# Optimization experiments

Hardware: AMD Instinct MI355X
Metric: run time of the kernel (lower is better)

Reference implementation:

```python
import jax, jax.numpy as jnp
import numpy as np

B, S, R, L, Z = 2048, 277, 80, 12, 56


def setup_inputs() -> dict:
    key = jax.random.key(0)
    k0, k1, k2, k3, k4, k5 = jax.random.split(key, 6)
    true_idx = jax.random.randint(k0, (B, S), 0, R)
    x = jax.nn.one_hot(true_idx, R, dtype=jnp.float32)            # one-hot true rules
    recon_x = jax.nn.softmax(jax.random.normal(k1, (B, S, R)), axis=-1)  # post-softmax probs
    mu = jax.random.normal(k2, (B, Z), dtype=jnp.float32)
    log_var = jax.random.normal(k3, (B, Z), dtype=jnp.float32)
    ind_to_lhs_ind = jax.random.randint(k4, (R,), 0, L)
    masks = (jax.random.uniform(k5, (L, R)) > 0.5).astype(jnp.float32)
    # a valid grammar always allows the true rule under its own LHS mask
    masks = masks.at[ind_to_lhs_ind, jnp.arange(R)].set(1.0)
    return {"x": x, "recon_x": recon_x, "mu": mu, "log_var": log_var,
            "masks": masks, "ind_to_lhs_ind": ind_to_lhs_ind}


def reference(x, recon_x, mu, log_var, masks, ind_to_lhs_ind):
    batch_size, seq_len, n_rules = x.shape
    z_size = mu.shape[1]
    # apply_masks: fused gather + mask + renormalize (replaces B*S python loop)
    true_rule = jnp.argmax(x, axis=-1)                 # [B,S]
    mask = masks[ind_to_lhs_ind[true_rule]]            # [B,S,R]
    x_resc = recon_x * mask
    out = x_resc / jnp.sum(x_resc, axis=-1, keepdims=True)
    # BCELoss(size_average=False): torch clamps log terms at -100
    log_p = jnp.clip(jnp.log(out), -100.0, None)
    log_1mp = jnp.clip(jnp.log1p(-out), -100.0, None)
    bce = -jnp.sum(x * log_p + (1.0 - x) * log_1mp) / (seq_len * batch_size)
    # sample_z == False branch: moment-matching error
    avg_mu = jnp.sum(mu, axis=0) / batch_size          # [Z]
    var = jnp.matmul(mu.T, mu) / batch_size            # [Z,Z]
    var_err = var - jnp.eye(z_size, dtype=mu.dtype)
    mom_err = jnp.sum(avg_mu * avg_mu) / z_size + jnp.sum(jnp.abs(var_err)) / (z_size * z_size)
    return bce + mom_err
```

## Files before the change

kernel.cpp:

```cpp
#include <hip/hip_runtime.h>
#include <math.h>

#define Bn 2048
#define Sn 277
#define Rn 80
#define Ln 12
#define Zn 56
#define NROWS (Bn * Sn)
#define ROWS_PER_BLK 64
#define NBLK_BCE (NROWS / ROWS_PER_BLK)
#define NMOM 32
#define MROWS (Bn / NMOM)
#define NBLK_TOT (NBLK_BCE + NMOM)

#define WS_CM  0
#define WS_BCE 1280
#define WS_VAR 36736
#define WS_AVG 49280

__device__ __forceinline__ float qsum4(float v) {
    int t = __builtin_amdgcn_update_dpp(0, __float_as_int(v), 0xB1, 0xF, 0xF, true);
    v += __int_as_float(t);
    t = __builtin_amdgcn_update_dpp(0, __float_as_int(v), 0x4E, 0xF, 0xF, true);
    v += __int_as_float(t);
    return v;
}

__global__ __launch_bounds__(256) void setup_kernel(
    const float* __restrict__ masks, const int* __restrict__ lhs, char* __restrict__ ws)
{
    unsigned* cmask_sw = (unsigned*)(ws + WS_CM);
    for (int idx = threadIdx.x; idx < Rn * 4; idx += 256) {
        const int r = idx >> 2, c = idx & 3;
        const int l = lhs[r];
        unsigned bits = 0u;
        for (int k = 0; k < 5; ++k)
            for (int comp = 0; comp < 4; ++comp) {
                const int j = 16 * k + 4 * c + comp;
                if (masks[l * Rn + j] > 0.5f) bits |= (1u << (4 * k + comp));
            }
        cmask_sw[idx] = bits;
    }
}

__global__ __launch_bounds__(256, 3) void main_kernel(
    const float* __restrict__ x, const float* __restrict__ recon,
    const float* __restrict__ mu, char* __restrict__ ws)
{
    __shared__ float4 ldsb[2688];
    const int tid = threadIdx.x;

    if (blockIdx.x < NMOM) {
        float* var_g = (float*)(ws + WS_VAR);
        float* avg_g = (float*)(ws + WS_AVG);
        float* sm = (float*)ldsb;
        const int m = blockIdx.x;
        const float* src = mu + (size_t)m * MROWS * Zn;
        for (int i = tid; i < MROWS * Zn; i += 256) sm[i] = src[i];
        __syncthreads();

        float acc[13];
        #pragma unroll
        for (int k = 0; k < 13; ++k) {
            const int p = tid + 256 * k;
            float a = 0.0f;
            if (p < Zn * Zn) {
                const int i = p / Zn, j = p - i * Zn;
                #pragma unroll 8
                for (int r = 0; r < MROWS; ++r) a = fmaf(sm[r * Zn + i], sm[r * Zn + j], a);
            }
            acc[k] = a;
        }
        #pragma unroll
        for (int k = 0; k < 13; ++k) {
            const int p = tid + 256 * k;
            if (p < Zn * Zn) atomicAdd(&var_g[p], acc[k]);
        }
        if (tid < Zn) {
            float s = 0.0f;
            #pragma unroll 8
            for (int r = 0; r < MROWS; ++r) s += sm[r * Zn + tid];
            atomicAdd(&avg_g[tid], s);
        }
        return;
    }

    const int bid = blockIdx.x - NMOM;
    const unsigned* cmask_sw = (const unsigned*)(ws + WS_CM);
    float* bce_partial = (float*)(ws + WS_BCE);

    const size_t base = (size_t)bid * (ROWS_PER_BLK * (Rn / 4));
    const float4* xg = (const float4*)x + base;
    const float4* rg = (const float4*)recon + base;

    float4 tv[10];
    #pragma unroll
    for (int i = 0; i < 5; ++i) tv[i]     = xg[256 * i + tid];
    #pragma unroll
    for (int i = 0; i < 5; ++i) tv[5 + i] = rg[256 * i + tid];
    #pragma unroll
    for (int i = 0; i < 5; ++i) {
        const int f = 256 * i + tid;
        const int row = f / 20, col = f - 20 * row;
        ldsb[row * 21 + col]        = tv[i];
        ldsb[1344 + row * 21 + col] = tv[5 + i];
    }
    __syncthreads();

    const int qq = tid >> 2;
    const int c  = tid & 3;
    const int sb = qq * 21 + c;

    float4 X[5], Rv[5];
    #pragma unroll
    for (int k = 0; k < 5; ++k) X[k]  = ldsb[sb + 4 * k];
    #pragma unroll
    for (int k = 0; k < 5; ++k) Rv[k] = ldsb[1344 + sb + 4 * k];

    auto dotc = [](const float4 v, float base_) {
        return fmaf(v.x, base_, fmaf(v.y, base_ + 1.f, fmaf(v.z, base_ + 2.f, v.w * (base_ + 3.f))));
    };

    float ss = 0.0f;
    {
        float dl = dotc(X[0], 0.f) + dotc(X[1], 16.f) + dotc(X[2], 32.f)
                 + dotc(X[3], 48.f) + dotc(X[4], 64.f);
        float xs = 0.f;
        #pragma unroll
        for (int k = 0; k < 5; ++k)
            xs += ((X[k].x + X[k].y) + (X[k].z + X[k].w));
        dl = fmaf((float)(4 * c), xs, dl);
        const int amax = (int)(qsum4(dl) + 0.5f);

        const unsigned bits = cmask_sw[(amax << 2) | c];

        float4 M[5];
        #pragma unroll
        for (int k = 0; k < 5; ++k) {
            M[k].x = ((bits >> (4 * k + 0)) & 1u) ? Rv[k].x : 0.f;
            M[k].y = ((bits >> (4 * k + 1)) & 1u) ? Rv[k].y : 0.f;
            M[k].z = ((bits >> (4 * k + 2)) & 1u) ? Rv[k].z : 0.f;
            M[k].w = ((bits >> (4 * k + 3)) & 1u) ? Rv[k].w : 0.f;
        }
        float dd = 0.f;
        #pragma unroll
        for (int k = 0; k < 5; ++k)
            dd += ((M[k].x + M[k].y) + (M[k].z + M[k].w));
        const float invd = __builtin_amdgcn_rcpf(qsum4(dd));

        const int ka = amax >> 4;
        const int ca = (amax >> 2) & 3;
        const int comp = amax & 3;
        const bool owner = (c == ca);

        float p = 1.0f;
        float ta = 1.0f;
        #pragma unroll
        for (int k = 0; k < 5; ++k) {
            const float t0 = fminf(M[k].x * invd, 1.f);
            const float t1 = fminf(M[k].y * invd, 1.f);
            const float t2 = fminf(M[k].z * invd, 1.f);
            const float t3 = fminf(M[k].w * invd, 1.f);
            p *= ((1.f - t0) * (1.f - t1)) * ((1.f - t2) * (1.f - t3));
            if (owner && k == ka)
                ta = (comp == 0) ? t0 : (comp == 1) ? t1 : (comp == 2) ? t2 : t3;
        }
        if (p > 0.0f) {
            ss += __builtin_amdgcn_logf(p) * 0.69314718055994531f;
        } else {
            #pragma unroll
            for (int k = 0; k < 5; ++k) {
                ss += fmaxf(__logf(1.f - fminf(M[k].x * invd, 1.f)), -100.f)
                    + fmaxf(__logf(1.f - fminf(M[k].y * invd, 1.f)), -100.f)
                    + fmaxf(__logf(1.f - fminf(M[k].z * invd, 1.f)), -100.f)
                    + fmaxf(__logf(1.f - fminf(M[k].w * invd, 1.f)), -100.f);
            }
        }
        if (owner)
            ss += fmaxf(__logf(ta), -100.f) - fmaxf(__logf(1.f - ta), -100.f);
    }

    ss = qsum4(ss);
    ss += __shfl_xor(ss, 4);
    ss += __shfl_xor(ss, 8);
    ss += __shfl_xor(ss, 16);
    ss += __shfl_xor(ss, 32);
    __syncthreads();
    float* smf = (float*)ldsb;
    if ((tid & 63) == 0) smf[tid >> 6] = ss;
    __syncthreads();
    if (tid == 0)
        bce_partial[bid] = (smf[0] + smf[1]) + (smf[2] + smf[3]);
}

__global__ __launch_bounds__(256) void finalize_kernel(
    const char* __restrict__ ws, float* __restrict__ out)
{
    const float* bce_partial = (const float*)(ws + WS_BCE);
    const float* var_g = (const float*)(ws + WS_VAR);
    const float* avg_g = (const float*)(ws + WS_AVG);
    __shared__ double sb[4];
    __shared__ float sv[4], sa[4];
    const int tid = threadIdx.x;

    double bsum = 0.0;
    for (int i = tid; i < NBLK_BCE; i += 256) bsum += (double)bce_partial[i];

    float vsum = 0.0f;
    for (int p = tid; p < Zn * Zn; p += 256) {
        const int i = p / Zn, j = p - i * Zn;
        const float e = var_g[p] * (1.0f / (float)Bn) - ((i == j) ? 1.0f : 0.0f);
        vsum += fabsf(e);
    }
    float asum = 0.0f;
    for (int z = tid; z < Zn; z += 256) { const float a = avg_g[z]; asum += a * a; }

    #pragma unroll
    for (int o = 32; o; o >>= 1) {
        bsum += __shfl_xor(bsum, o);
        vsum += __shfl_xor(vsum, o);
        asum += __shfl_xor(asum, o);
    }
    if ((tid & 63) == 0) { const int w = tid >> 6; sb[w] = bsum; sv[w] = vsum; sa[w] = asum; }
    __syncthreads();
    if (tid == 0) {
        const double tb = (sb[0] + sb[1]) + (sb[2] + sb[3]);
        const double tv = (double)((sv[0] + sv[1]) + (sv[2] + sv[3]));
        const double ta = (double)((sa[0] + sa[1]) + (sa[2] + sa[3]));
        const double bce = -tb / ((double)Sn * (double)Bn);
        const double mom = ta / ((double)Bn * (double)Bn * (double)Zn)
                         + tv / ((double)Zn * (double)Zn);
        out[0] = (float)(bce + mom);
    }
}

extern "C" void kernel_launch(void* const* d_in, const int* in_sizes, int n_in,
                              void* d_out, int out_size, void* d_ws, size_t ws_size,
                              hipStream_t stream)
{
    const float* x     = (const float*)d_in[0];
    const float* recon = (const float*)d_in[1];
    const float* mu    = (const float*)d_in[2];
    const float* masks = (const float*)d_in[4];
    const int*   lhs   = (const int*)d_in[5];
    float* out = (float*)d_out;
    char* ws = (char*)d_ws;

    hipMemsetAsync(ws + WS_VAR, 0, 12544 + 224, stream);
    setup_kernel<<<1, 256, 0, stream>>>(masks, lhs, ws);
    main_kernel<<<NBLK_TOT, 256, 0, stream>>>(x, recon, mu, ws);
    finalize_kernel<<<1, 256, 0, stream>>>(ws, out);
}
```

Before: 377.2 us.

## Drop LDS staging, load rows directly and loop four row-chunks per block

The BCE path no longer stages x and recon through shared memory with a transpose and barriers. Each quad of threads now loads its row's float4 values straight from global memory, and each block walks four chunks of 64 rows. Per-wave partial sums are written directly instead of going through a shared-memory block reduction. Launch bounds rise to 8 blocks per CU, and the moment blocks do their atomics inside the loop to free registers. The aim is to remove LDS traffic and syncs and raise occupancy, at the cost of less perfectly coalesced global loads.

```diff
diff --git a/kernel.cpp b/kernel.cpp
--- a/kernel.cpp
+++ b/kernel.cpp
@@ -7,11 +7,12 @@
 #define Ln 12
 #define Zn 56
 #define NROWS (Bn * Sn)
-#define ROWS_PER_BLK 64
-#define NBLK_BCE (NROWS / ROWS_PER_BLK)
+#define NBLK_BCE 2216
+#define ITERS 4
 #define NMOM 32
 #define MROWS (Bn / NMOM)
 #define NBLK_TOT (NBLK_BCE + NMOM)
+#define NWAVE_BCE (NBLK_BCE * 4)
 
 #define WS_CM  0
 #define WS_BCE 1280
@@ -43,38 +44,31 @@
     }
 }
 
-__global__ __launch_bounds__(256, 3) void main_kernel(
+__global__ __launch_bounds__(256, 8) void main_kernel(
     const float* __restrict__ x, const float* __restrict__ recon,
     const float* __restrict__ mu, char* __restrict__ ws)
 {
-    __shared__ float4 ldsb[2688];
     const int tid = threadIdx.x;
 
     if (blockIdx.x < NMOM) {
+        __shared__ float sm[MROWS * Zn];
         float* var_g = (float*)(ws + WS_VAR);
         float* avg_g = (float*)(ws + WS_AVG);
-        float* sm = (float*)ldsb;
         const int m = blockIdx.x;
         const float* src = mu + (size_t)m * MROWS * Zn;
         for (int i = tid; i < MROWS * Zn; i += 256) sm[i] = src[i];
         __syncthreads();
 
-        float acc[13];
-        #pragma unroll
+        #pragma unroll 1
         for (int k = 0; k < 13; ++k) {
             const int p = tid + 256 * k;
-            float a = 0.0f;
             if (p < Zn * Zn) {
                 const int i = p / Zn, j = p - i * Zn;
+                float a = 0.0f;
                 #pragma unroll 8
                 for (int r = 0; r < MROWS; ++r) a = fmaf(sm[r * Zn + i], sm[r * Zn + j], a);
+                atomicAdd(&var_g[p], a);
             }
-            acc[k] = a;
-        }
-        #pragma unroll
-        for (int k = 0; k < 13; ++k) {
-            const int p = tid + 256 * k;
-            if (p < Zn * Zn) atomicAdd(&var_g[p], acc[k]);
         }
         if (tid < Zn) {
             float s = 0.0f;
@@ -89,40 +83,26 @@
     const unsigned* cmask_sw = (const unsigned*)(ws + WS_CM);
     float* bce_partial = (float*)(ws + WS_BCE);
 
-    const size_t base = (size_t)bid * (ROWS_PER_BLK * (Rn / 4));
-    const float4* xg = (const float4*)x + base;
-    const float4* rg = (const float4*)recon + base;
-
-    float4 tv[10];
-    #pragma unroll
-    for (int i = 0; i < 5; ++i) tv[i]     = xg[256 * i + tid];
-    #pragma unroll
-    for (int i = 0; i < 5; ++i) tv[5 + i] = rg[256 * i + tid];
-    #pragma unroll
-    for (int i = 0; i < 5; ++i) {
-        const int f = 256 * i + tid;
-        const int row = f / 20, col = f - 20 * row;
-        ldsb[row * 21 + col]        = tv[i];
-        ldsb[1344 + row * 21 + col] = tv[5 + i];
-    }
-    __syncthreads();
-
-    const int qq = tid >> 2;
-    const int c  = tid & 3;
-    const int sb = qq * 21 + c;
-
-    float4 X[5], Rv[5];
-    #pragma unroll
-    for (int k = 0; k < 5; ++k) X[k]  = ldsb[sb + 4 * k];
-    #pragma unroll
-    for (int k = 0; k < 5; ++k) Rv[k] = ldsb[1344 + sb + 4 * k];
+    const int q = tid >> 2;
+    const int c = tid & 3;
+    const float4* xp = (const float4*)x;
+    const float4* rp = (const float4*)recon;
+    int off = (bid * 256 + q) * 20 + c;
 
     auto dotc = [](const float4 v, float base_) {
         return fmaf(v.x, base_, fmaf(v.y, base_ + 1.f, fmaf(v.z, base_ + 2.f, v.w * (base_ + 3.f))));
     };
 
     float ss = 0.0f;
-    {
+    #pragma unroll 1
+    for (int it = 0; it < ITERS; ++it, off += 64 * 20) {
+        float4 X[5], Rv[5];
+        #pragma unroll
+        for (int k = 0; k < 5; ++k) X[k]  = xp[off + 4 * k];
+        #pragma unroll
+        for (int k = 0; k < 5; ++k) Rv[k] = rp[off + 4 * k];
+        __builtin_amdgcn_sched_barrier(0);
+
         float dl = dotc(X[0], 0.f) + dotc(X[1], 16.f) + dotc(X[2], 32.f)
                  + dotc(X[3], 48.f) + dotc(X[4], 64.f);
         float xs = 0.f;
@@ -134,18 +114,17 @@
 
         const unsigned bits = cmask_sw[(amax << 2) | c];
 
-        float4 M[5];
         #pragma unroll
         for (int k = 0; k < 5; ++k) {
-            M[k].x = ((bits >> (4 * k + 0)) & 1u) ? Rv[k].x : 0.f;
-            M[k].y = ((bits >> (4 * k + 1)) & 1u) ? Rv[k].y : 0.f;
-            M[k].z = ((bits >> (4 * k + 2)) & 1u) ? Rv[k].z : 0.f;
-            M[k].w = ((bits >> (4 * k + 3)) & 1u) ? Rv[k].w : 0.f;
+            Rv[k].x = ((bits >> (4 * k + 0)) & 1u) ? Rv[k].x : 0.f;
+            Rv[k].y = ((bits >> (4 * k + 1)) & 1u) ? Rv[k].y : 0.f;
+            Rv[k].z = ((bits >> (4 * k + 2)) & 1u) ? Rv[k].z : 0.f;
+            Rv[k].w = ((bits >> (4 * k + 3)) & 1u) ? Rv[k].w : 0.f;
         }
         float dd = 0.f;
         #pragma unroll
         for (int k = 0; k < 5; ++k)
-            dd += ((M[k].x + M[k].y) + (M[k].z + M[k].w));
+            dd += ((Rv[k].x + Rv[k].y) + (Rv[k].z + Rv[k].w));
         const float invd = __builtin_amdgcn_rcpf(qsum4(dd));
 
         const int ka = amax >> 4;
@@ -157,10 +136,10 @@
         float ta = 1.0f;
         #pragma unroll
         for (int k = 0; k < 5; ++k) {
-            const float t0 = fminf(M[k].x * invd, 1.f);
-            const float t1 = fminf(M[k].y * invd, 1.f);
-            const float t2 = fminf(M[k].z * invd, 1.f);
-            const float t3 = fminf(M[k].w * invd, 1.f);
+            const float t0 = fminf(Rv[k].x * invd, 1.f);
+            const float t1 = fminf(Rv[k].y * invd, 1.f);
+            const float t2 = fminf(Rv[k].z * invd, 1.f);
+            const float t3 = fminf(Rv[k].w * invd, 1.f);
             p *= ((1.f - t0) * (1.f - t1)) * ((1.f - t2) * (1.f - t3));
             if (owner && k == ka)
                 ta = (comp == 0) ? t0 : (comp == 1) ? t1 : (comp == 2) ? t2 : t3;
@@ -170,10 +149,10 @@
         } else {
             #pragma unroll
             for (int k = 0; k < 5; ++k) {
-                ss += fmaxf(__logf(1.f - fminf(M[k].x * invd, 1.f)), -100.f)
-                    + fmaxf(__logf(1.f - fminf(M[k].y * invd, 1.f)), -100.f)
-                    + fmaxf(__logf(1.f - fminf(M[k].z * invd, 1.f)), -100.f)
-                    + fmaxf(__logf(1.f - fminf(M[k].w * invd, 1.f)), -100.f);
+                ss += fmaxf(__logf(1.f - fminf(Rv[k].x * invd, 1.f)), -100.f)
+                    + fmaxf(__logf(1.f - fminf(Rv[k].y * invd, 1.f)), -100.f)
+                    + fmaxf(__logf(1.f - fminf(Rv[k].z * invd, 1.f)), -100.f)
+                    + fmaxf(__logf(1.f - fminf(Rv[k].w * invd, 1.f)), -100.f);
             }
         }
         if (owner)
@@ -185,12 +164,8 @@
     ss += __shfl_xor(ss, 8);
     ss += __shfl_xor(ss, 16);
     ss += __shfl_xor(ss, 32);
-    __syncthreads();
-    float* smf = (float*)ldsb;
-    if ((tid & 63) == 0) smf[tid >> 6] = ss;
-    __syncthreads();
-    if (tid == 0)
-        bce_partial[bid] = (smf[0] + smf[1]) + (smf[2] + smf[3]);
+    if ((tid & 63) == 0)
+        bce_partial[bid * 4 + (tid >> 6)] = ss;
 }
 
 __global__ __launch_bounds__(256) void finalize_kernel(
@@ -204,7 +179,7 @@
     const int tid = threadIdx.x;
 
     double bsum = 0.0;
-    for (int i = tid; i < NBLK_BCE; i += 256) bsum += (double)bce_partial[i];
+    for (int i = tid; i < NWAVE_BCE; i += 256) bsum += (double)bce_partial[i];
 
     float vsum = 0.0f;
     for (int p = tid; p < Zn * Zn; p += 256) {
```

After: 388.9 us. +3.1%, slower.
